# Kernel optimization log

Hardware: AMD Instinct MI355X
Metric: run time of the kernel (lower is better)

The kernel has to match this reference:

```python
import jax, jax.numpy as jnp
import numpy as np

B, C, H, W = 8, 256, 64, 64
D = C // 8  # query/key channels


def setup_inputs() -> dict:
    key = jax.random.key(0)
    ks = jax.random.split(key, 7)
    s = 0.05
    x = jax.random.normal(ks[0], (B, C, H, W), dtype=jnp.float32)
    Wq = jax.random.normal(ks[1], (D, C), dtype=jnp.float32) * s
    bq = jax.random.normal(ks[2], (D,), dtype=jnp.float32) * s
    Wk = jax.random.normal(ks[3], (D, C), dtype=jnp.float32) * s
    bk = jax.random.normal(ks[4], (D,), dtype=jnp.float32) * s
    Wv = jax.random.normal(ks[5], (C, C), dtype=jnp.float32) * s
    bv = jax.random.normal(ks[6], (C,), dtype=jnp.float32) * s
    return {"x": x, "Wq": Wq, "bq": bq, "Wk": Wk, "bk": bk, "Wv": Wv, "bv": bv}


def reference(x, Wq, bq, Wk, bk, Wv, bv):
    b, c, h, w = x.shape
    n = h * w
    xf = x.reshape(b, c, n)  # (B, C, HW)
    # 1x1 convs == per-pixel linear projections
    q = jnp.einsum('dc,bcn->bdn', Wq, xf) + bq[None, :, None]  # (B, D, HW)
    k = jnp.einsum('dc,bcn->bdn', Wk, xf) + bk[None, :, None]  # (B, D, HW)
    v = jnp.einsum('ec,bcn->ben', Wv, xf) + bv[None, :, None]  # (B, C, HW)
    # attention[b, n, m] = sum_d q[b,d,n] * k[b,d,m]  (no 1/sqrt(d) scaling)
    attn = jax.nn.softmax(jnp.einsum('bdn,bdm->bnm', q, k), axis=-1)
    # out[b,c,n] = sum_m v[b,c,m] * attn[b,n,m]  (v @ attn^T)
    out = jnp.einsum('bcm,bnm->bcn', v, attn)
    return out.reshape(b, c, h, w) + x
```

## Files before the change

### kernel.cpp

```cpp
#include <hip/hip_runtime.h>
#include <stdint.h>

#define BN 4096
#define NCH 256
#define DQ 32

typedef _Float16 half8  __attribute__((ext_vector_type(8)));
typedef _Float16 half4  __attribute__((ext_vector_type(4)));
typedef float   floatx4  __attribute__((ext_vector_type(4)));
typedef float   floatx16 __attribute__((ext_vector_type(16)));

typedef __attribute__((address_space(1))) const void g1_void;
typedef __attribute__((address_space(3))) void l3_void;

#define LOG2E 1.44269504088896f
#define EXP2F(x) __builtin_amdgcn_exp2f(x)
#define LOG2F(x) __builtin_amdgcn_logf(x)

__global__ __launch_bounds__(256) void convert_w(
    const float* __restrict__ Wq, const float* __restrict__ Wk,
    const float* __restrict__ Wv, _Float16* __restrict__ W16)
{
    int e4 = (blockIdx.x * 256 + threadIdx.x) * 4;
    float4 v;
    if (e4 < 8192)        v = *(const float4*)&Wq[e4];
    else if (e4 < 16384) {
        v = *(const float4*)&Wk[e4 - 8192];
        v.x *= LOG2E; v.y *= LOG2E; v.z *= LOG2E; v.w *= LOG2E;
    }
    else                  v = *(const float4*)&Wv[e4 - 16384];
    half4 h = { (_Float16)v.x, (_Float16)v.y, (_Float16)v.z, (_Float16)v.w };
    *(half4*)&W16[e4] = h;
}

__global__ __launch_bounds__(512) void proj_kernel(
    const float* __restrict__ x, const _Float16* __restrict__ W16,
    const float* __restrict__ bq, const float* __restrict__ bk,
    const float* __restrict__ bv,
    _Float16* __restrict__ qT, _Float16* __restrict__ kT,
    _Float16* __restrict__ vb)
{
    const int t  = threadIdx.x;
    const int n0 = blockIdx.x * 128;
    const int b  = blockIdx.y;

    __shared__ __align__(16) _Float16 xTl[128 * 256];

#pragma unroll
    for (int p = 0; p < 2; ++p) {
        const int kb = p * 128 + (t >> 5) * 8;
        const int n4 = (t & 31) * 4;
        float4 xr[8];
#pragma unroll
        for (int i = 0; i < 8; ++i)
            xr[i] = *(const float4*)&x[((size_t)b * NCH + kb + i) * BN + n0 + n4];
        const float* xf = (const float*)xr;
#pragma unroll
        for (int j = 0; j < 4; ++j) {
            const int n = n4 + j;
            half8 hv;
#pragma unroll
            for (int i = 0; i < 8; ++i) hv[i] = (_Float16)xf[i * 4 + j];
            const int phys = (kb >> 3) ^ ((n >> 2) & 31);
            *(half8*)&xTl[n * 256 + phys * 8] = hv;
        }
    }
    __syncthreads();

    const int lane  = t & 63;
    const int w     = t >> 6;
    const int col32 = lane & 31;
    const int h     = lane >> 5;
    const int nc    = w & 3;
    const int job   = w >> 2;

    const _Float16* Wq16 = W16;
    const _Float16* Wk16 = W16 + 8192;
    const _Float16* Wv16 = W16 + 16384;

#define XFRAG(ks) (*(const half8*)&xTl[(nc * 32 + col32) * 256 + \
        (((ks) * 2 + h) ^ (((nc * 32 + col32) >> 2) & 31)) * 8])

    if (job == 0) {
        const float bqv = bq[col32];
        const float bkv = bk[col32] * LOG2E;
        floatx16 aq, ak2;
#pragma unroll
        for (int r = 0; r < 16; ++r) { aq[r] = 0.0f; ak2[r] = 0.0f; }
#pragma unroll
        for (int ks = 0; ks < 16; ++ks) {
            half8 xa = XFRAG(ks);
            half8 wqf = *(const half8*)&Wq16[col32 * 256 + ks * 16 + h * 8];
            half8 wkf = *(const half8*)&Wk16[col32 * 256 + ks * 16 + h * 8];
            aq  = __builtin_amdgcn_mfma_f32_32x32x16_f16(xa, wqf, aq, 0, 0, 0);
            ak2 = __builtin_amdgcn_mfma_f32_32x32x16_f16(xa, wkf, ak2, 0, 0, 0);
        }
#pragma unroll
        for (int r = 0; r < 16; ++r) {
            const int n = n0 + nc * 32 + (r & 3) + 8 * (r >> 2) + 4 * h;
            qT[((size_t)b * BN + n) * DQ + col32] = (_Float16)(aq[r] + bqv);
            kT[((size_t)b * BN + n) * DQ + col32] = (_Float16)(ak2[r] + bkv);
        }
    }

    const int rg_lo = (job == 0) ? 0 : 3;
    const int rg_hi = (job == 0) ? 3 : 8;
    for (int rg = rg_lo; rg < rg_hi; ++rg) {
        floatx16 av;
#pragma unroll
        for (int r = 0; r < 16; ++r) av[r] = 0.0f;
#pragma unroll
        for (int ks = 0; ks < 16; ++ks) {
            half8 xb  = XFRAG(ks);
            half8 wvf = *(const half8*)&Wv16[(rg * 32 + col32) * 256 + ks * 16 + h * 8];
            av = __builtin_amdgcn_mfma_f32_32x32x16_f16(wvf, xb, av, 0, 0, 0);
        }
#pragma unroll
        for (int r = 0; r < 16; ++r) {
            const int c = rg * 32 + (r & 3) + 8 * (r >> 2) + 4 * h;
            vb[((size_t)b * NCH + c) * BN + n0 + nc * 32 + col32] =
                (_Float16)(av[r] + bv[c]);
        }
    }
#undef XFRAG
}

__global__ __launch_bounds__(256, 3) void flash_kernel(
    const _Float16* __restrict__ qT, const _Float16* __restrict__ kT,
    const _Float16* __restrict__ vb,
    _Float16* __restrict__ Op, float* __restrict__ Ml, int KPS)
{
    const int t    = threadIdx.x;
    const int lane = t & 63;
    const int w    = t >> 6;
    const int n0   = blockIdx.x * 64;
    const int kh   = blockIdx.y;
    const int b    = blockIdx.z;
    const int kbase = kh * KPS;
    const int iters = (min(KPS, BN - kbase)) >> 6;

    __shared__ __align__(16) _Float16 vs[NCH * 64];
    __shared__ __align__(16) _Float16 Ps[64 * 64];
    __shared__ float alph_s[64];
    __shared__ float l_s[64];

    const int col   = lane & 15;
    const int q4    = lane >> 4;
    const int col32 = lane & 31;
    const int h     = lane >> 5;

    const _Float16* kp = kT + (size_t)b * BN * DQ;
    const _Float16* vp = vb + (size_t)b * NCH * BN;

    half8 bqf = *(const half8*)&qT[((size_t)b * BN + n0 + w * 16 + col) * DQ + q4 * 8];

    floatx16 acc[2][2];
#pragma unroll
    for (int ct = 0; ct < 2; ++ct)
#pragma unroll
        for (int nt = 0; nt < 2; ++nt)
#pragma unroll
            for (int r = 0; r < 16; ++r) acc[ct][nt][r] = 0.0f;

    float m_i = -1e30f, l_i = 0.0f;

    const int sc_loc = lane >> 3;
    const int s_log  = (lane & 7) ^ (sc_loc & 7);
    half8 ak[4];
#pragma unroll
    for (int mt = 0; mt < 4; ++mt)
        ak[mt] = *(const half8*)&kp[(size_t)(kbase + mt * 16 + col) * DQ + q4 * 8];
#pragma unroll
    for (int j = 0; j < 8; ++j) {
        const int c = w * 64 + j * 8 + sc_loc;
        __builtin_amdgcn_global_load_lds(
            (g1_void*)&vp[(size_t)c * BN + kbase + s_log * 8],
            (l3_void*)&vs[(w * 64 + j * 8) * 64], 16, 0, 0);
    }

    for (int it = 0; it < iters; ++it) {
        const int mc = kbase + it * 64;

        floatx4 sf[4];
#pragma unroll
        for (int mt = 0; mt < 4; ++mt) {
            floatx4 z = { 0.0f, 0.0f, 0.0f, 0.0f };
            sf[mt] = __builtin_amdgcn_mfma_f32_16x16x32_f16(ak[mt], bqf, z, 0, 0, 0);
        }

        float cmax = -1e30f;
#pragma unroll
        for (int mt = 0; mt < 4; ++mt)
#pragma unroll
            for (int r = 0; r < 4; ++r) cmax = fmaxf(cmax, sf[mt][r]);
        cmax = fmaxf(cmax, __shfl_xor(cmax, 16));
        cmax = fmaxf(cmax, __shfl_xor(cmax, 32));
        const float mn = (cmax > m_i + 8.0f) ? cmax : m_i;
        float al = EXP2F(m_i - mn);
        float csum = 0.0f;
        half4 pk[4];
#pragma unroll
        for (int mt = 0; mt < 4; ++mt) {
            float p0 = EXP2F(sf[mt][0] - mn);
            float p1 = EXP2F(sf[mt][1] - mn);
            float p2 = EXP2F(sf[mt][2] - mn);
            float p3 = EXP2F(sf[mt][3] - mn);
            csum += p0 + p1 + p2 + p3;
            pk[mt] = (half4){ (_Float16)p0, (_Float16)p1, (_Float16)p2, (_Float16)p3 };
        }
        csum += __shfl_xor(csum, 16);
        csum += __shfl_xor(csum, 32);
        l_i = l_i * al + csum;
        m_i = mn;

        {
            const int n = w * 16 + col;
#pragma unroll
            for (int mt = 0; mt < 4; ++mt) {
                const int p_log = 2 * mt + (q4 >> 1);
                const int p_phys = p_log ^ (n & 7);
                *(half4*)((char*)&Ps[n * 64] + p_phys * 16 + (q4 & 1) * 8) = pk[mt];
            }
            if (q4 == 0) alph_s[n] = al;
        }

        __syncthreads();

        float a0 = alph_s[col32];
        float a1 = alph_s[32 + col32];
        if (!__all((a0 == 1.0f) && (a1 == 1.0f))) {
#pragma unroll
            for (int ct = 0; ct < 2; ++ct)
#pragma unroll
                for (int r = 0; r < 16; ++r) {
                    acc[ct][0][r] *= a0;
                    acc[ct][1][r] *= a1;
                }
        }

#pragma unroll
        for (int ks = 0; ks < 4; ++ks) {
            const int p_log = 2 * ks + h;
            half8 bp0 = *(const half8*)((char*)&Ps[col32 * 64] + (p_log ^ (col32 & 7)) * 16);
            half8 bp1 = *(const half8*)((char*)&Ps[(32 + col32) * 64] + (p_log ^ (col32 & 7)) * 16);
#pragma unroll
            for (int ct = 0; ct < 2; ++ct) {
                const int c = w * 64 + ct * 32 + col32;
                half8 av = *(const half8*)((char*)&vs[c * 64] + ((p_log ^ (c & 7)) * 16));
                acc[ct][0] = __builtin_amdgcn_mfma_f32_32x32x16_f16(av, bp0, acc[ct][0], 0, 0, 0);
                acc[ct][1] = __builtin_amdgcn_mfma_f32_32x32x16_f16(av, bp1, acc[ct][1], 0, 0, 0);
            }
        }

        __syncthreads();

        if (it + 1 < iters) {
            const int mcn = mc + 64;
#pragma unroll
            for (int mt = 0; mt < 4; ++mt)
                ak[mt] = *(const half8*)&kp[(size_t)(mcn + mt * 16 + col) * DQ + q4 * 8];
#pragma unroll
            for (int j = 0; j < 8; ++j) {
                const int c = w * 64 + j * 8 + sc_loc;
                __builtin_amdgcn_global_load_lds(
                    (g1_void*)&vp[(size_t)c * BN + mcn + s_log * 8],
                    (l3_void*)&vs[(w * 64 + j * 8) * 64], 16, 0, 0);
            }
        }
    }

    if (q4 == 0) {
        const int n = w * 16 + col;
        l_s[n] = l_i;
        Ml[(size_t)(kh * 8 + b) * BN + n0 + n] = m_i + LOG2F(l_i);
    }
    __syncthreads();
    const float li0 = 1.0f / l_s[col32];
    const float li1 = 1.0f / l_s[32 + col32];

    _Float16* Opp = Op + (size_t)(kh * 8 + b) * NCH * BN;
#pragma unroll
    for (int ct = 0; ct < 2; ++ct)
#pragma unroll
        for (int nt = 0; nt < 2; ++nt) {
            const float li = nt ? li1 : li0;
#pragma unroll
            for (int r = 0; r < 16; ++r) {
                int row = (r & 3) + 8 * (r >> 2) + 4 * h;
                int c = w * 64 + ct * 32 + row;
                Opp[(size_t)c * BN + n0 + nt * 32 + col32] = (_Float16)(acc[ct][nt][r] * li);
            }
        }
}

__global__ __launch_bounds__(256) void combine_kernel(
    const _Float16* __restrict__ Op, const float* __restrict__ Ml,
    const float* __restrict__ x, float* __restrict__ out, int nsplit)
{
    const int n  = (blockIdx.x * 256 + threadIdx.x) * 4;
    const int c0 = blockIdx.y * 16;
    const int b  = blockIdx.z;

    floatx4 zr[3];
    floatx4 Z = { -1e30f, -1e30f, -1e30f, -1e30f };
    for (int s = 0; s < nsplit; ++s) {
        zr[s] = *(const floatx4*)&Ml[(size_t)(s * 8 + b) * BN + n];
#pragma unroll
        for (int j = 0; j < 4; ++j) Z[j] = fmaxf(Z[j], zr[s][j]);
    }
    float f[3][4];
    floatx4 lsum = { 0.0f, 0.0f, 0.0f, 0.0f };
    for (int s = 0; s < nsplit; ++s)
#pragma unroll
        for (int j = 0; j < 4; ++j) { f[s][j] = EXP2F(zr[s][j] - Z[j]); lsum[j] += f[s][j]; }
#pragma unroll
    for (int j = 0; j < 4; ++j) lsum[j] = 1.0f / lsum[j];
    for (int s = 0; s < nsplit; ++s)
#pragma unroll
        for (int j = 0; j < 4; ++j) f[s][j] *= lsum[j];

#pragma unroll 4
    for (int ci = 0; ci < 16; ++ci) {
        const int c = c0 + ci;
        const size_t off = ((size_t)b * NCH + c) * BN + n;
        const size_t po = (size_t)c * BN + n;
        floatx4 ov = { 0.0f, 0.0f, 0.0f, 0.0f };
        for (int s = 0; s < nsplit; ++s) {
            half4 hv = *(const half4*)&Op[(size_t)(s * 8 + b) * NCH * BN + po];
#pragma unroll
            for (int j = 0; j < 4; ++j) ov[j] += (float)hv[j] * f[s][j];
        }
        floatx4 xv = *(const floatx4*)&x[off];
#pragma unroll
        for (int j = 0; j < 4; ++j) ov[j] += xv[j];
        *(floatx4*)&out[off] = ov;
    }
}

extern "C" void kernel_launch(void* const* d_in, const int* in_sizes, int n_in,
                              void* d_out, int out_size, void* d_ws, size_t ws_size,
                              hipStream_t stream)
{
    const float* x  = (const float*)d_in[0];
    const float* Wq = (const float*)d_in[1];
    const float* bq = (const float*)d_in[2];
    const float* Wk = (const float*)d_in[3];
    const float* bk = (const float*)d_in[4];
    const float* Wv = (const float*)d_in[5];
    const float* bv = (const float*)d_in[6];
    float* out = (float*)d_out;

    _Float16* ws = (_Float16*)d_ws;
    _Float16* W16 = ws;
    _Float16* qT  = W16 + 81920;
    _Float16* kT  = qT + (size_t)8 * BN * DQ;
    _Float16* vb  = kT + (size_t)8 * BN * DQ;
    _Float16* Op  = vb + (size_t)8 * NCH * BN;

    const size_t baseElems = 81920 + (size_t)2 * 8 * BN * DQ + (size_t)8 * NCH * BN;
    const size_t opElems3  = (size_t)3 * 8 * NCH * BN;
    const size_t mlBytes   = (size_t)24 * BN * sizeof(float);
    const size_t need3     = (baseElems + opElems3) * 2 + mlBytes + 256;
    const int nsplit = (ws_size >= need3) ? 3 : 2;
    const int KPS    = (nsplit == 3) ? 1408 : 2048;

    float* Ml = (float*)(Op + (size_t)nsplit * 8 * NCH * BN);

    convert_w<<<dim3(80), 256, 0, stream>>>(Wq, Wk, Wv, W16);
    proj_kernel<<<dim3(32, 8), 512, 0, stream>>>(x, W16, bq, bk, bv, qT, kT, vb);
    flash_kernel<<<dim3(64, nsplit, 8), 256, 0, stream>>>(qT, kT, vb, Op, Ml, KPS);
    combine_kernel<<<dim3(4, 16, 8), 256, 0, stream>>>(Op, Ml, x, out, nsplit);
}
```

Baseline: 247.1 us.

## Prefetch K earlier, add MFMA priority hints, packed f16 convert, widen combine

Inside the flash loop, the next K fragments are now loaded right after the QK^T MFMAs instead of after the barrier, so their latency overlaps the softmax and PV work. s_setprio raises wave priority around both MFMA blocks. Probability conversion switches to packed round-toward-zero f16 conversion. The combine kernel now processes 8 pixels per thread with half the grid, giving wider loads. The trade-offs are more live registers from the early prefetch, and rounding that differs slightly from round-to-nearest.

After: 246.0 us. Within noise of the previous version (-0.4%).

```diff
diff --git a/kernel.cpp b/kernel.cpp
--- a/kernel.cpp
+++ b/kernel.cpp
@@ -7,6 +7,7 @@
 
 typedef _Float16 half8  __attribute__((ext_vector_type(8)));
 typedef _Float16 half4  __attribute__((ext_vector_type(4)));
+typedef _Float16 half2  __attribute__((ext_vector_type(2)));
 typedef float   floatx4  __attribute__((ext_vector_type(4)));
 typedef float   floatx16 __attribute__((ext_vector_type(16)));
 
@@ -182,10 +183,19 @@
         const int mc = kbase + it * 64;
 
         floatx4 sf[4];
+        __builtin_amdgcn_s_setprio(1);
 #pragma unroll
         for (int mt = 0; mt < 4; ++mt) {
             floatx4 z = { 0.0f, 0.0f, 0.0f, 0.0f };
             sf[mt] = __builtin_amdgcn_mfma_f32_16x16x32_f16(ak[mt], bqf, z, 0, 0, 0);
+        }
+        __builtin_amdgcn_s_setprio(0);
+
+        if (it + 1 < iters) {
+            const int mcn = mc + 64;
+#pragma unroll
+            for (int mt = 0; mt < 4; ++mt)
+                ak[mt] = *(const half8*)&kp[(size_t)(mcn + mt * 16 + col) * DQ + q4 * 8];
         }
 
         float cmax = -1e30f;
@@ -206,7 +216,12 @@
             float p2 = EXP2F(sf[mt][2] - mn);
             float p3 = EXP2F(sf[mt][3] - mn);
             csum += p0 + p1 + p2 + p3;
-            pk[mt] = (half4){ (_Float16)p0, (_Float16)p1, (_Float16)p2, (_Float16)p3 };
+            half2 q01 = __builtin_bit_cast(half2, __builtin_amdgcn_cvt_pkrtz(p0, p1));
+            half2 q23 = __builtin_bit_cast(half2, __builtin_amdgcn_cvt_pkrtz(p2, p3));
+            half4 pkv;
+            pkv[0] = q01[0]; pkv[1] = q01[1];
+            pkv[2] = q23[0]; pkv[3] = q23[1];
+            pk[mt] = pkv;
         }
         csum += __shfl_xor(csum, 16);
         csum += __shfl_xor(csum, 32);
@@ -238,6 +253,7 @@
                 }
         }
 
+        __builtin_amdgcn_s_setprio(1);
 #pragma unroll
         for (int ks = 0; ks < 4; ++ks) {
             const int p_log = 2 * ks + h;
@@ -251,14 +267,12 @@
                 acc[ct][1] = __builtin_amdgcn_mfma_f32_32x32x16_f16(av, bp1, acc[ct][1], 0, 0, 0);
             }
         }
+        __builtin_amdgcn_s_setprio(0);
 
         __syncthreads();
 
         if (it + 1 < iters) {
             const int mcn = mc + 64;
-#pragma unroll
-            for (int mt = 0; mt < 4; ++mt)
-                ak[mt] = *(const half8*)&kp[(size_t)(mcn + mt * 16 + col) * DQ + q4 * 8];
 #pragma unroll
             for (int j = 0; j < 8; ++j) {
                 const int c = w * 64 + j * 8 + sc_loc;
@@ -297,43 +311,55 @@
     const _Float16* __restrict__ Op, const float* __restrict__ Ml,
     const float* __restrict__ x, float* __restrict__ out, int nsplit)
 {
-    const int n  = (blockIdx.x * 256 + threadIdx.x) * 4;
+    const int n  = (blockIdx.x * 256 + threadIdx.x) * 8;
     const int c0 = blockIdx.y * 16;
     const int b  = blockIdx.z;
 
-    floatx4 zr[3];
-    floatx4 Z = { -1e30f, -1e30f, -1e30f, -1e30f };
+    float f[3][8];
+    float Z[8];
+#pragma unroll
+    for (int j = 0; j < 8; ++j) Z[j] = -1e30f;
     for (int s = 0; s < nsplit; ++s) {
-        zr[s] = *(const floatx4*)&Ml[(size_t)(s * 8 + b) * BN + n];
-#pragma unroll
-        for (int j = 0; j < 4; ++j) Z[j] = fmaxf(Z[j], zr[s][j]);
-    }
-    float f[3][4];
-    floatx4 lsum = { 0.0f, 0.0f, 0.0f, 0.0f };
+        const float* mlp = &Ml[(size_t)(s * 8 + b) * BN + n];
+        floatx4 z0 = *(const floatx4*)mlp;
+        floatx4 z1 = *(const floatx4*)(mlp + 4);
+#pragma unroll
+        for (int j = 0; j < 4; ++j) { f[s][j] = z0[j]; f[s][4 + j] = z1[j]; }
+#pragma unroll
+        for (int j = 0; j < 8; ++j) Z[j] = fmaxf(Z[j], f[s][j]);
+    }
+    float lsum[8];
+#pragma unroll
+    for (int j = 0; j < 8; ++j) lsum[j] = 0.0f;
     for (int s = 0; s < nsplit; ++s)
 #pragma unroll
-        for (int j = 0; j < 4; ++j) { f[s][j] = EXP2F(zr[s][j] - Z[j]); lsum[j] += f[s][j]; }
-#pragma unroll
-    for (int j = 0; j < 4; ++j) lsum[j] = 1.0f / lsum[j];
+        for (int j = 0; j < 8; ++j) { f[s][j] = EXP2F(f[s][j] - Z[j]); lsum[j] += f[s][j]; }
+#pragma unroll
+    for (int j = 0; j < 8; ++j) lsum[j] = 1.0f / lsum[j];
     for (int s = 0; s < nsplit; ++s)
 #pragma unroll
-        for (int j = 0; j < 4; ++j) f[s][j] *= lsum[j];
-
-#pragma unroll 4
+        for (int j = 0; j < 8; ++j) f[s][j] *= lsum[j];
+
+#pragma unroll 2
     for (int ci = 0; ci < 16; ++ci) {
         const int c = c0 + ci;
         const size_t off = ((size_t)b * NCH + c) * BN + n;
         const size_t po = (size_t)c * BN + n;
-        floatx4 ov = { 0.0f, 0.0f, 0.0f, 0.0f };
+        float ov[8];
+#pragma unroll
+        for (int j = 0; j < 8; ++j) ov[j] = 0.0f;
         for (int s = 0; s < nsplit; ++s) {
-            half4 hv = *(const half4*)&Op[(size_t)(s * 8 + b) * NCH * BN + po];
-#pragma unroll
-            for (int j = 0; j < 4; ++j) ov[j] += (float)hv[j] * f[s][j];
-        }
-        floatx4 xv = *(const floatx4*)&x[off];
-#pragma unroll
-        for (int j = 0; j < 4; ++j) ov[j] += xv[j];
-        *(floatx4*)&out[off] = ov;
+            half8 hv = *(const half8*)&Op[(size_t)(s * 8 + b) * NCH * BN + po];
+#pragma unroll
+            for (int j = 0; j < 8; ++j) ov[j] += (float)hv[j] * f[s][j];
+        }
+        floatx4 x0 = *(const floatx4*)&x[off];
+        floatx4 x1 = *(const floatx4*)&x[off + 4];
+        floatx4 o0, o1;
+#pragma unroll
+        for (int j = 0; j < 4; ++j) { o0[j] = ov[j] + x0[j]; o1[j] = ov[4 + j] + x1[j]; }
+        *(floatx4*)&out[off] = o0;
+        *(floatx4*)&out[off + 4] = o1;
     }
 }
 
@@ -369,5 +395,5 @@
     convert_w<<<dim3(80), 256, 0, stream>>>(Wq, Wk, Wv, W16);
     proj_kernel<<<dim3(32, 8), 512, 0, stream>>>(x, W16, bq, bk, bv, qT, kT, vb);
     flash_kernel<<<dim3(64, nsplit, 8), 256, 0, stream>>>(qT, kT, vb, Op, Ml, KPS);
-    combine_kernel<<<dim3(4, 16, 8), 256, 0, stream>>>(Op, Ml, x, out, nsplit);
-}
+    combine_kernel<<<dim3(2, 16, 8), 256, 0, stream>>>(Op, Ml, x, out, nsplit);
+}
```
